# Kernel optimization log

Hardware: AMD Instinct MI355X
Metric: run time of the kernel (lower is better)

Reference implementation:

```python
import jax, jax.numpy as jnp
import numpy as np

EMBED_DIM = 1024
NUM_HEADS = 16
HEAD_DIM = EMBED_DIM // NUM_HEADS


def setup_inputs() -> dict:
    key = jax.random.key(0)
    ks = jax.random.split(key, 5)
    B, S, E = 2, 2048, EMBED_DIM
    # xavier-uniform-ish scale for square linear weights
    lim = float(np.sqrt(6.0 / (E + E)))
    x = jax.random.normal(ks[0], (B, S, E), dtype=jnp.float32)
    Wq = jax.random.uniform(ks[1], (E, E), jnp.float32, -lim, lim)
    Wk = jax.random.uniform(ks[2], (E, E), jnp.float32, -lim, lim)
    Wv = jax.random.uniform(ks[3], (E, E), jnp.float32, -lim, lim)
    Wo = jax.random.uniform(ks[4], (E, E), jnp.float32, -lim, lim)
    z = jnp.zeros((E,), jnp.float32)
    return {"x": x, "Wq": Wq, "bq": z, "Wk": Wk, "bk": z,
            "Wv": Wv, "bv": z, "Wo": Wo, "bo": z}


def reference(x, Wq, bq, Wk, bk, Wv, bv, Wo, bo):
    B, S, E = x.shape
    H, Dh = NUM_HEADS, HEAD_DIM
    # Linear projections (torch Linear: y = x @ W.T + b)
    q = (x @ Wq.T + bq).reshape(B, S, H, Dh).transpose(0, 2, 1, 3)  # [B,H,S,Dh]
    k = (x @ Wk.T + bk).reshape(B, S, H, Dh).transpose(0, 2, 1, 3)
    v = (x @ Wv.T + bv).reshape(B, S, H, Dh).transpose(0, 2, 1, 3)
    # NOTE: module scales by 1/head_dim (not 1/sqrt(head_dim)) — faithful.
    logits = jnp.einsum('bhqd,bhkd->bhqk', q, k) / Dh  # [B,H,S,S]
    attn = jax.nn.softmax(logits, axis=-1)
    vals = jnp.einsum('bhqk,bhkd->bhqd', attn, v)      # [B,H,S,Dh]
    vals = vals.transpose(0, 2, 1, 3).reshape(B, S, E)
    out = vals @ Wo.T + bo
    return out
```

## Files before the change

kernel.cpp:

```cpp
#include <hip/hip_runtime.h>
#include <hip/hip_bf16.h>

#define EDIM 1024
#define NH   16
#define DH   64
#define BB   2
#define SS   2048
#define MM   (BB*SS)

typedef unsigned short u16;
typedef unsigned int   u32;
typedef __attribute__((ext_vector_type(4)))  float f32x4;
typedef __attribute__((ext_vector_type(16))) float f32x16;
typedef __attribute__((ext_vector_type(8)))  short s16x8;

__device__ __forceinline__ u16 f2bf(float x) {
    __hip_bfloat16 b = __float2bfloat16(x);
    return *(u16*)&b;
}
__device__ __forceinline__ u32 cvtpk(float lo, float hi_) {
    u32 r;
    asm("v_cvt_pk_bf16_f32 %0, %1, %2" : "=v"(r) : "v"(lo), "v"(hi_));
    return r;
}
__device__ __forceinline__ void swap32(u32& a, u32& b) {
    asm("v_permlane32_swap_b32 %0, %1" : "+v"(a), "+v"(b));
}

__device__ __forceinline__ void gload16(const void* g, void* l) {
    __builtin_amdgcn_global_load_lds(
        (const __attribute__((address_space(1))) unsigned int*)g,
        (__attribute__((address_space(3))) unsigned int*)l, 16, 0, 0);
}

__global__ __launch_bounds__(256) void convert_all(const float* __restrict__ x,
                                                   const float* __restrict__ Wq,
                                                   const float* __restrict__ Wk,
                                                   const float* __restrict__ Wv,
                                                   const float* __restrict__ Wo,
                                                   u16* __restrict__ xh,
                                                   u16* __restrict__ wqkv,
                                                   u16* __restrict__ woh)
{
    const int i = blockIdx.x * 256 + threadIdx.x;
    const float* src; ushort4* dst; int off;
    if (i < 1048576)      { src = x;  dst = (ushort4*)xh;   off = i; }
    else if (i < 1310720) { src = Wq; dst = (ushort4*)wqkv; off = i - 1048576; }
    else if (i < 1572864) { src = Wk; dst = (ushort4*)wqkv; off = i - 1310720 + 262144; }
    else if (i < 1835008) { src = Wv; dst = (ushort4*)wqkv; off = i - 1572864 + 524288; }
    else                  { src = Wo; dst = (ushort4*)woh;  off = i - 1835008; }
    const int so = (i < 1048576) ? i
                 : (i < 1310720) ? (i - 1048576)
                 : (i < 1572864) ? (i - 1310720)
                 : (i < 1835008) ? (i - 1572864) : (i - 1835008);
    const float4 v = ((const float4*)src)[so];
    ushort4 h;
    h.x = f2bf(v.x); h.y = f2bf(v.y); h.z = f2bf(v.z); h.w = f2bf(v.w);
    dst[off] = h;
}

__global__ __launch_bounds__(256) void gemm_qkv(const u16* __restrict__ A,
                                                const u16* __restrict__ B,
                                                const float* __restrict__ bq,
                                                const float* __restrict__ bk,
                                                const float* __restrict__ bv,
                                                u16* __restrict__ qb,
                                                u16* __restrict__ kb,
                                                u16* __restrict__ vT)
{
    __shared__ __align__(16) u16 As[128][32];
    __shared__ __align__(16) u16 Bs[128][32];

    const int tid  = threadIdx.x;
    const int lane = tid & 63, wid = tid >> 6;
    const int wm = wid >> 1, wn = wid & 1;
    const int swz   = (blockIdx.x & 7) * 96 + (blockIdx.x >> 3);
    const int m0 = (swz & 31) * 128;
    const int n0 = (swz >> 5) * 128;

    f32x4 acc[4][4];
    #pragma unroll
    for (int i = 0; i < 4; ++i)
        #pragma unroll
        for (int j = 0; j < 4; ++j) acc[i][j] = f32x4{0.f, 0.f, 0.f, 0.f};

    const int lrow0 = tid >> 2;
    const int lcol  = (tid & 3) * 8;

    for (int k0 = 0; k0 < 1024; k0 += 32) {
        __syncthreads();
        gload16(A + (size_t)(m0 + lrow0)      * 1024 + k0 + lcol, (char*)As + wid * 1024);
        gload16(A + (size_t)(m0 + 64 + lrow0) * 1024 + k0 + lcol, (char*)As + 4096 + wid * 1024);
        gload16(B + (size_t)(n0 + lrow0)      * 1024 + k0 + lcol, (char*)Bs + wid * 1024);
        gload16(B + (size_t)(n0 + 64 + lrow0) * 1024 + k0 + lcol, (char*)Bs + 4096 + wid * 1024);
        __syncthreads();

        s16x8 af[4], bf[4];
        #pragma unroll
        for (int i = 0; i < 4; ++i) {
            af[i] = *(const s16x8*)&As[wm * 64 + i * 16 + (lane & 15)][(lane >> 4) * 8];
            bf[i] = *(const s16x8*)&Bs[wn * 64 + i * 16 + (lane & 15)][(lane >> 4) * 8];
        }
        #pragma unroll
        for (int i = 0; i < 4; ++i)
            #pragma unroll
            for (int j = 0; j < 4; ++j)
                acc[i][j] = __builtin_amdgcn_mfma_f32_16x16x32_bf16(af[i], bf[j], acc[i][j], 0, 0, 0);
    }

    if (n0 < 1024) {
        #pragma unroll
        for (int i = 0; i < 4; ++i) {
            const int mbase = m0 + wm * 64 + i * 16 + ((lane >> 4) * 4);
            #pragma unroll
            for (int j = 0; j < 4; ++j) {
                const int n = n0 + wn * 64 + j * 16 + (lane & 15);
                const float bias = bq[n];
                const int h_ = n >> 6, d_ = n & 63;
                #pragma unroll
                for (int r = 0; r < 4; ++r) {
                    const int m = mbase + r;
                    const int b_ = m >> 11, s_ = m & 2047;
                    qb[((size_t)(b_ * NH + h_) * SS + s_) * DH + d_] = f2bf(acc[i][j][r] + bias);
                }
            }
        }
    } else if (n0 < 2048) {
        #pragma unroll
        for (int i = 0; i < 4; ++i) {
            const int mbase = m0 + wm * 64 + i * 16 + ((lane >> 4) * 4);
            #pragma unroll
            for (int j = 0; j < 4; ++j) {
                const int n = n0 + wn * 64 + j * 16 + (lane & 15);
                const float bias = bk[n - 1024];
                const int h_ = (n >> 6) & 15, d_ = n & 63;
                #pragma unroll
                for (int r = 0; r < 4; ++r) {
                    const int m = mbase + r;
                    const int b_ = m >> 11, s_ = m & 2047;
                    kb[((size_t)(b_ * NH + h_) * SS + s_) * DH + d_] = f2bf(acc[i][j][r] + bias);
                }
            }
        }
    } else {
        #pragma unroll
        for (int i = 0; i < 4; ++i) {
            const int mbase = m0 + wm * 64 + i * 16 + ((lane >> 4) * 4);
            #pragma unroll
            for (int j = 0; j < 4; ++j) {
                const int n = n0 + wn * 64 + j * 16 + (lane & 15);
                const float bias = bv[n - 2048];
                const int hd = n - 2048;
                #pragma unroll
                for (int r = 0; r < 4; ++r) {
                    const int m = mbase + r;
                    const int b_ = m >> 11, s_ = m & 2047;
                    vT[((size_t)(b_ * EDIM) + hd) * SS + s_] = f2bf(acc[i][j][r] + bias);
                }
            }
        }
    }
}

__global__ __launch_bounds__(256) void gemm_out(const u16* __restrict__ A,
                                                const u16* __restrict__ B,
                                                const float* __restrict__ bo,
                                                float* __restrict__ out)
{
    __shared__ __align__(16) u16 As[64][32];
    __shared__ __align__(16) u16 Bs[128][32];

    const int tid  = threadIdx.x;
    const int lane = tid & 63, wid = tid >> 6;
    const int wm = wid >> 1, wn = wid & 1;
    const int swz = (blockIdx.x & 7) * 64 + (blockIdx.x >> 3);
    const int m0 = (swz & 63) * 64;
    const int n0 = (swz >> 6) * 128;

    f32x4 acc[2][4];
    #pragma unroll
    for (int i = 0; i < 2; ++i)
        #pragma unroll
        for (int j = 0; j < 4; ++j) acc[i][j] = f32x4{0.f, 0.f, 0.f, 0.f};

    const int lrow0 = tid >> 2;
    const int lcol  = (tid & 3) * 8;

    for (int k0 = 0; k0 < 1024; k0 += 32) {
        __syncthreads();
        gload16(A + (size_t)(m0 + lrow0)      * 1024 + k0 + lcol, (char*)As + wid * 1024);
        gload16(B + (size_t)(n0 + lrow0)      * 1024 + k0 + lcol, (char*)Bs + wid * 1024);
        gload16(B + (size_t)(n0 + 64 + lrow0) * 1024 + k0 + lcol, (char*)Bs + 4096 + wid * 1024);
        __syncthreads();

        s16x8 af[2], bf[4];
        #pragma unroll
        for (int i = 0; i < 2; ++i)
            af[i] = *(const s16x8*)&As[wm * 32 + i * 16 + (lane & 15)][(lane >> 4) * 8];
        #pragma unroll
        for (int j = 0; j < 4; ++j)
            bf[j] = *(const s16x8*)&Bs[wn * 64 + j * 16 + (lane & 15)][(lane >> 4) * 8];
        #pragma unroll
        for (int i = 0; i < 2; ++i)
            #pragma unroll
            for (int j = 0; j < 4; ++j)
                acc[i][j] = __builtin_amdgcn_mfma_f32_16x16x32_bf16(af[i], bf[j], acc[i][j], 0, 0, 0);
    }

    #pragma unroll
    for (int i = 0; i < 2; ++i) {
        const int mbase = m0 + wm * 32 + i * 16 + ((lane >> 4) * 4);
        #pragma unroll
        for (int j = 0; j < 4; ++j) {
            const int n = n0 + wn * 64 + j * 16 + (lane & 15);
            #pragma unroll
            for (int r = 0; r < 4; ++r)
                out[(size_t)(mbase + r) * EDIM + n] = acc[i][j][r] + bo[n];
        }
    }
}

__global__ __launch_bounds__(256) void attn_mfma(const u16* __restrict__ q,
                                                 const u16* __restrict__ k,
                                                 const u16* __restrict__ vT,
                                                 u16* __restrict__ valsh)
{
    __shared__ __align__(16) u16 kt[128][64];
    __shared__ __align__(16) u16 vt[64][128];

    const int tid = threadIdx.x, lane = tid & 63, wid = tid >> 6;
    const int lq = lane & 31, hi = lane >> 5;
    const int swz = (blockIdx.x & 7) * 64 + (blockIdx.x >> 3);
    const int bh = swz >> 4, qt = swz & 15;
    const int b = bh >> 4, h = bh & 15;

    const u16* qg = q + ((size_t)bh * SS + qt * 128 + wid * 32 + lq) * DH + hi * 8;
    s16x8 qf[4];
    #pragma unroll
    for (int ks = 0; ks < 4; ++ks) qf[ks] = *(const s16x8*)(qg + ks * 16);

    f32x16 acc_o[2];
    #pragma unroll
    for (int db = 0; db < 2; ++db)
        #pragma unroll
        for (int r = 0; r < 16; ++r) acc_o[db][r] = 0.f;
    float rs = 0.f;

    const char* kbh = (const char*)(k + (size_t)bh * SS * DH);
    const char* vbh = (const char*)(vT + ((size_t)b * EDIM + h * DH) * SS);

    #pragma unroll 1
    for (int c0 = 0; c0 < SS; c0 += 128) {
        #pragma unroll
        for (int i = 0; i < 4; ++i) {
            const int flat = i * 256 + tid;
            const int row = flat >> 3, u = flat & 7;
            gload16(kbh + (size_t)(c0 + row) * 128 + ((u ^ (row & 7)) << 4),
                    (char*)kt + (i * 256 + wid * 64) * 16);
        }
        #pragma unroll
        for (int i = 0; i < 4; ++i) {
            const int flat = i * 256 + tid;
            const int row = flat >> 4, u = flat & 15;
            gload16(vbh + (size_t)row * (SS * 2) + (size_t)c0 * 2 + ((u ^ (row & 15)) << 4),
                    (char*)vt + (i * 256 + wid * 64) * 16);
        }
        __syncthreads();

        #pragma unroll
        for (int kb = 0; kb < 4; ++kb) {
            f32x16 sc;
            #pragma unroll
            for (int r = 0; r < 16; ++r) sc[r] = 0.f;
            const int krow = kb * 32 + lq;
            __builtin_amdgcn_s_setprio(1);
            #pragma unroll
            for (int ks = 0; ks < 4; ++ks) {
                const int u = (ks * 2 + hi) ^ (krow & 7);
                const s16x8 kf = *(const s16x8*)((const char*)kt + krow * 128 + u * 16);
                sc = __builtin_amdgcn_mfma_f32_32x32x16_bf16(kf, qf[ks], sc, 0, 0, 0);
            }
            __builtin_amdgcn_s_setprio(0);

            #pragma unroll
            for (int r = 0; r < 16; ++r) {
                sc[r] = __builtin_amdgcn_exp2f(sc[r] * 0.0225421209f);
                rs += sc[r];
            }

            u32 w0 = cvtpk(sc[0],  sc[1]),  w1 = cvtpk(sc[2],  sc[3]);
            u32 w2 = cvtpk(sc[4],  sc[5]),  w3 = cvtpk(sc[6],  sc[7]);
            u32 w4 = cvtpk(sc[8],  sc[9]),  w5 = cvtpk(sc[10], sc[11]);
            u32 w6 = cvtpk(sc[12], sc[13]), w7 = cvtpk(sc[14], sc[15]);
            swap32(w0, w2);
            swap32(w1, w3);
            swap32(w4, w6);
            swap32(w5, w7);
            union { u32 w[4]; s16x8 v; } pa0, pa1;
            pa0.w[0] = w0; pa0.w[1] = w1; pa0.w[2] = w2; pa0.w[3] = w3;
            pa1.w[0] = w4; pa1.w[1] = w5; pa1.w[2] = w6; pa1.w[3] = w7;

            __builtin_amdgcn_s_setprio(1);
            #pragma unroll
            for (int t = 0; t < 2; ++t) {
                const s16x8 pat = t ? pa1.v : pa0.v;
                const int kst = kb * 2 + t;
                #pragma unroll
                for (int db = 0; db < 2; ++db) {
                    const int vrow = db * 32 + lq;
                    const int u = (kst * 2 + hi) ^ (vrow & 15);
                    const s16x8 vf = *(const s16x8*)((const char*)vt + vrow * 256 + u * 16);
                    acc_o[db] = __builtin_amdgcn_mfma_f32_32x32x16_bf16(pat, vf, acc_o[db], 0, 0, 0);
                }
            }
            __builtin_amdgcn_s_setprio(0);
        }
        __syncthreads();
    }

    const float rsf = rs + __shfl_xor(rs, 32, 64);
    const float inv = 1.f / rsf;
    float iv[16];
    #pragma unroll
    for (int r = 0; r < 16; ++r)
        iv[r] = __shfl(inv, (r & 3) + 8 * (r >> 2) + 4 * hi, 64);

    #pragma unroll
    for (int db = 0; db < 2; ++db)
        #pragma unroll
        for (int r = 0; r < 16; ++r) {
            const int srow = qt * 128 + wid * 32 + (r & 3) + 8 * (r >> 2) + 4 * hi;
            const int col  = h * 64 + db * 32 + lq;
            valsh[(size_t)(b * SS + srow) * EDIM + col] = f2bf(acc_o[db][r] * iv[r]);
        }
}

extern "C" void kernel_launch(void* const* d_in, const int* in_sizes, int n_in,
                              void* d_out, int out_size, void* d_ws, size_t ws_size,
                              hipStream_t stream)
{
    const float* x  = (const float*)d_in[0];
    const float* Wq = (const float*)d_in[1];
    const float* bq = (const float*)d_in[2];
    const float* Wk = (const float*)d_in[3];
    const float* bk = (const float*)d_in[4];
    const float* Wv = (const float*)d_in[5];
    const float* bv = (const float*)d_in[6];
    const float* Wo = (const float*)d_in[7];
    const float* bo = (const float*)d_in[8];
    float* out = (float*)d_out;

    u16* W = (u16*)d_ws;
    const size_t M1 = 1024 * 1024;
    u16* xh    = W;
    u16* wqkv  = W + 4  * M1;
    u16* woh   = W + 7  * M1;
    u16* qbuf  = W + 8  * M1;
    u16* kbuf  = W + 12 * M1;
    u16* vbufT = W + 16 * M1;
    u16* valsh = W + 20 * M1;

    convert_all<<<dim3(8192), 256, 0, stream>>>(x, Wq, Wk, Wv, Wo, xh, wqkv, woh);

    gemm_qkv<<<dim3(768), 256, 0, stream>>>(xh, wqkv, bq, bk, bv, qbuf, kbuf, vbufT);

    attn_mfma<<<dim3(BB * NH * (SS / 128)), 256, 0, stream>>>(qbuf, kbuf, vbufT, valsh);

    gemm_out<<<dim3(512), 256, 0, stream>>>(valsh, woh, bo, out);
}
```

Before: 205.2 us.

## Double-buffer LDS tiles in GEMMs and attention with swizzled, deeper K tiles

Adds two-stage LDS double buffering to the QKV projection, output projection and attention kernels, so the async global-to-LDS loads for the next tile are issued before computing on the current one. Each iteration then needs one barrier instead of two. The GEMMs also widen the K step from 32 to 64 and XOR-swizzle the LDS layout to avoid bank conflicts. In exchange, LDS use doubles, which may lower occupancy, and the swizzle adds some address arithmetic.

```diff
diff --git a/kernel.cpp b/kernel.cpp
--- a/kernel.cpp
+++ b/kernel.cpp
@@ -68,45 +68,71 @@
                                                 u16* __restrict__ kb,
                                                 u16* __restrict__ vT)
 {
-    __shared__ __align__(16) u16 As[128][32];
-    __shared__ __align__(16) u16 Bs[128][32];
+    __shared__ __align__(16) u16 As[2][128][64];
+    __shared__ __align__(16) u16 Bs[2][128][64];
 
     const int tid  = threadIdx.x;
     const int lane = tid & 63, wid = tid >> 6;
     const int wm = wid >> 1, wn = wid & 1;
-    const int swz   = (blockIdx.x & 7) * 96 + (blockIdx.x >> 3);
+    const int swz = (blockIdx.x & 7) * 96 + (blockIdx.x >> 3);
     const int m0 = (swz & 31) * 128;
     const int n0 = (swz >> 5) * 128;
 
+    const char* Abase = (const char*)(A + (size_t)m0 * 1024);
+    const char* Bbase = (const char*)(B + (size_t)n0 * 1024);
+
     f32x4 acc[4][4];
     #pragma unroll
     for (int i = 0; i < 4; ++i)
         #pragma unroll
         for (int j = 0; j < 4; ++j) acc[i][j] = f32x4{0.f, 0.f, 0.f, 0.f};
 
-    const int lrow0 = tid >> 2;
-    const int lcol  = (tid & 3) * 8;
-
-    for (int k0 = 0; k0 < 1024; k0 += 32) {
+    auto stage = [&](int buf, int k0) {
+        #pragma unroll
+        for (int i = 0; i < 4; ++i) {
+            const int flat = i * 256 + tid;
+            const int row = flat >> 3, u = flat & 7;
+            const size_t so = (size_t)row * 2048 + (size_t)k0 * 2 + ((u ^ (row & 7)) << 4);
+            gload16(Abase + so, (char*)As + buf * 16384 + (i * 256 + wid * 64) * 16);
+        }
+        #pragma unroll
+        for (int i = 0; i < 4; ++i) {
+            const int flat = i * 256 + tid;
+            const int row = flat >> 3, u = flat & 7;
+            const size_t so = (size_t)row * 2048 + (size_t)k0 * 2 + ((u ^ (row & 7)) << 4);
+            gload16(Bbase + so, (char*)Bs + buf * 16384 + (i * 256 + wid * 64) * 16);
+        }
+    };
+    auto compute = [&](int buf) {
+        const char* Ab = (const char*)As + buf * 16384;
+        const char* Bb = (const char*)Bs + buf * 16384;
+        #pragma unroll
+        for (int kk = 0; kk < 2; ++kk) {
+            s16x8 af[4], bfr[4];
+            #pragma unroll
+            for (int i = 0; i < 4; ++i) {
+                const int rowA = wm * 64 + i * 16 + (lane & 15);
+                af[i] = *(const s16x8*)(Ab + rowA * 128 + (((kk * 4 + (lane >> 4)) ^ (rowA & 7)) << 4));
+                const int rowB = wn * 64 + i * 16 + (lane & 15);
+                bfr[i] = *(const s16x8*)(Bb + rowB * 128 + (((kk * 4 + (lane >> 4)) ^ (rowB & 7)) << 4));
+            }
+            #pragma unroll
+            for (int i = 0; i < 4; ++i)
+                #pragma unroll
+                for (int j = 0; j < 4; ++j)
+                    acc[i][j] = __builtin_amdgcn_mfma_f32_16x16x32_bf16(af[i], bfr[j], acc[i][j], 0, 0, 0);
+        }
+    };
+
+    stage(0, 0);
+    __syncthreads();
+    #pragma unroll 1
+    for (int t = 0; t < 15; ++t) {
+        stage((t & 1) ^ 1, (t + 1) * 64);
+        compute(t & 1);
         __syncthreads();
-        gload16(A + (size_t)(m0 + lrow0)      * 1024 + k0 + lcol, (char*)As + wid * 1024);
-        gload16(A + (size_t)(m0 + 64 + lrow0) * 1024 + k0 + lcol, (char*)As + 4096 + wid * 1024);
-        gload16(B + (size_t)(n0 + lrow0)      * 1024 + k0 + lcol, (char*)Bs + wid * 1024);
-        gload16(B + (size_t)(n0 + 64 + lrow0) * 1024 + k0 + lcol, (char*)Bs + 4096 + wid * 1024);
-        __syncthreads();
-
-        s16x8 af[4], bf[4];
-        #pragma unroll
-        for (int i = 0; i < 4; ++i) {
-            af[i] = *(const s16x8*)&As[wm * 64 + i * 16 + (lane & 15)][(lane >> 4) * 8];
-            bf[i] = *(const s16x8*)&Bs[wn * 64 + i * 16 + (lane & 15)][(lane >> 4) * 8];
-        }
-        #pragma unroll
-        for (int i = 0; i < 4; ++i)
-            #pragma unroll
-            for (int j = 0; j < 4; ++j)
-                acc[i][j] = __builtin_amdgcn_mfma_f32_16x16x32_bf16(af[i], bf[j], acc[i][j], 0, 0, 0);
     }
+    compute(1);
 
     if (n0 < 1024) {
         #pragma unroll
@@ -167,8 +193,8 @@
                                                 const float* __restrict__ bo,
                                                 float* __restrict__ out)
 {
-    __shared__ __align__(16) u16 As[64][32];
-    __shared__ __align__(16) u16 Bs[128][32];
+    __shared__ __align__(16) u16 As[2][64][64];
+    __shared__ __align__(16) u16 Bs[2][128][64];
 
     const int tid  = threadIdx.x;
     const int lane = tid & 63, wid = tid >> 6;
@@ -177,35 +203,64 @@
     const int m0 = (swz & 63) * 64;
     const int n0 = (swz >> 6) * 128;
 
+    const char* Abase = (const char*)(A + (size_t)m0 * 1024);
+    const char* Bbase = (const char*)(B + (size_t)n0 * 1024);
+
     f32x4 acc[2][4];
     #pragma unroll
     for (int i = 0; i < 2; ++i)
         #pragma unroll
         for (int j = 0; j < 4; ++j) acc[i][j] = f32x4{0.f, 0.f, 0.f, 0.f};
 
-    const int lrow0 = tid >> 2;
-    const int lcol  = (tid & 3) * 8;
-
-    for (int k0 = 0; k0 < 1024; k0 += 32) {
+    auto stage = [&](int buf, int k0) {
+        #pragma unroll
+        for (int i = 0; i < 2; ++i) {
+            const int flat = i * 256 + tid;
+            const int row = flat >> 3, u = flat & 7;
+            const size_t so = (size_t)row * 2048 + (size_t)k0 * 2 + ((u ^ (row & 7)) << 4);
+            gload16(Abase + so, (char*)As + buf * 8192 + (i * 256 + wid * 64) * 16);
+        }
+        #pragma unroll
+        for (int i = 0; i < 4; ++i) {
+            const int flat = i * 256 + tid;
+            const int row = flat >> 3, u = flat & 7;
+            const size_t so = (size_t)row * 2048 + (size_t)k0 * 2 + ((u ^ (row & 7)) << 4);
+            gload16(Bbase + so, (char*)Bs + buf * 16384 + (i * 256 + wid * 64) * 16);
+        }
+    };
+    auto compute = [&](int buf) {
+        const char* Ab = (const char*)As + buf * 8192;
+        const char* Bb = (const char*)Bs + buf * 16384;
+        #pragma unroll
+        for (int kk = 0; kk < 2; ++kk) {
+            s16x8 af[2], bfr[4];
+            #pragma unroll
+            for (int i = 0; i < 2; ++i) {
+                const int rowA = wm * 32 + i * 16 + (lane & 15);
+                af[i] = *(const s16x8*)(Ab + rowA * 128 + (((kk * 4 + (lane >> 4)) ^ (rowA & 7)) << 4));
+            }
+            #pragma unroll
+            for (int j = 0; j < 4; ++j) {
+                const int rowB = wn * 64 + j * 16 + (lane & 15);
+                bfr[j] = *(const s16x8*)(Bb + rowB * 128 + (((kk * 4 + (lane >> 4)) ^ (rowB & 7)) << 4));
+            }
+            #pragma unroll
+            for (int i = 0; i < 2; ++i)
+                #pragma unroll
+                for (int j = 0; j < 4; ++j)
+                    acc[i][j] = __builtin_amdgcn_mfma_f32_16x16x32_bf16(af[i], bfr[j], acc[i][j], 0, 0, 0);
+        }
+    };
+
+    stage(0, 0);
+    __syncthreads();
+    #pragma unroll 1
+    for (int t = 0; t < 15; ++t) {
+        stage((t & 1) ^ 1, (t + 1) * 64);
+        compute(t & 1);
         __syncthreads();
-        gload16(A + (size_t)(m0 + lrow0)      * 1024 + k0 + lcol, (char*)As + wid * 1024);
-        gload16(B + (size_t)(n0 + lrow0)      * 1024 + k0 + lcol, (char*)Bs + wid * 1024);
-        gload16(B + (size_t)(n0 + 64 + lrow0) * 1024 + k0 + lcol, (char*)Bs + 4096 + wid * 1024);
-        __syncthreads();
-
-        s16x8 af[2], bf[4];
-        #pragma unroll
-        for (int i = 0; i < 2; ++i)
-            af[i] = *(const s16x8*)&As[wm * 32 + i * 16 + (lane & 15)][(lane >> 4) * 8];
-        #pragma unroll
-        for (int j = 0; j < 4; ++j)
-            bf[j] = *(const s16x8*)&Bs[wn * 64 + j * 16 + (lane & 15)][(lane >> 4) * 8];
-        #pragma unroll
-        for (int i = 0; i < 2; ++i)
-            #pragma unroll
-            for (int j = 0; j < 4; ++j)
-                acc[i][j] = __builtin_amdgcn_mfma_f32_16x16x32_bf16(af[i], bf[j], acc[i][j], 0, 0, 0);
     }
+    compute(1);
 
     #pragma unroll
     for (int i = 0; i < 2; ++i) {
@@ -225,8 +280,8 @@
                                                  const u16* __restrict__ vT,
                                                  u16* __restrict__ valsh)
 {
-    __shared__ __align__(16) u16 kt[128][64];
-    __shared__ __align__(16) u16 vt[64][128];
+    __shared__ __align__(16) u16 kt[2][128][64];
+    __shared__ __align__(16) u16 vt[2][64][128];
 
     const int tid = threadIdx.x, lane = tid & 63, wid = tid >> 6;
     const int lq = lane & 31, hi = lane >> 5;
@@ -249,23 +304,32 @@
     const char* kbh = (const char*)(k + (size_t)bh * SS * DH);
     const char* vbh = (const char*)(vT + ((size_t)b * EDIM + h * DH) * SS);
 
-    #pragma unroll 1
-    for (int c0 = 0; c0 < SS; c0 += 128) {
+    auto stage = [&](int buf, int c0) {
         #pragma unroll
         for (int i = 0; i < 4; ++i) {
             const int flat = i * 256 + tid;
             const int row = flat >> 3, u = flat & 7;
             gload16(kbh + (size_t)(c0 + row) * 128 + ((u ^ (row & 7)) << 4),
-                    (char*)kt + (i * 256 + wid * 64) * 16);
+                    (char*)kt + buf * 16384 + (i * 256 + wid * 64) * 16);
         }
         #pragma unroll
         for (int i = 0; i < 4; ++i) {
             const int flat = i * 256 + tid;
             const int row = flat >> 4, u = flat & 15;
             gload16(vbh + (size_t)row * (SS * 2) + (size_t)c0 * 2 + ((u ^ (row & 15)) << 4),
-                    (char*)vt + (i * 256 + wid * 64) * 16);
-        }
-        __syncthreads();
+                    (char*)vt + buf * 16384 + (i * 256 + wid * 64) * 16);
+        }
+    };
+
+    stage(0, 0);
+    __syncthreads();
+
+    int buf = 0;
+    #pragma unroll 1
+    for (int c = 0; c < 16; ++c) {
+        if (c < 15) stage(buf ^ 1, (c + 1) * 128);
+        const char* ktb = (const char*)kt + buf * 16384;
+        const char* vtb = (const char*)vt + buf * 16384;
 
         #pragma unroll
         for (int kb = 0; kb < 4; ++kb) {
@@ -277,7 +341,7 @@
             #pragma unroll
             for (int ks = 0; ks < 4; ++ks) {
                 const int u = (ks * 2 + hi) ^ (krow & 7);
-                const s16x8 kf = *(const s16x8*)((const char*)kt + krow * 128 + u * 16);
+                const s16x8 kf = *(const s16x8*)(ktb + krow * 128 + u * 16);
                 sc = __builtin_amdgcn_mfma_f32_32x32x16_bf16(kf, qf[ks], sc, 0, 0, 0);
             }
             __builtin_amdgcn_s_setprio(0);
@@ -309,13 +373,14 @@
                 for (int db = 0; db < 2; ++db) {
                     const int vrow = db * 32 + lq;
                     const int u = (kst * 2 + hi) ^ (vrow & 15);
-                    const s16x8 vf = *(const s16x8*)((const char*)vt + vrow * 256 + u * 16);
+                    const s16x8 vf = *(const s16x8*)(vtb + vrow * 256 + u * 16);
                     acc_o[db] = __builtin_amdgcn_mfma_f32_32x32x16_bf16(pat, vf, acc_o[db], 0, 0, 0);
                 }
             }
             __builtin_amdgcn_s_setprio(0);
         }
         __syncthreads();
+        buf ^= 1;
     }
 
     const float rsf = rs + __shfl_xor(rs, 32, 64);
```

Result: slower. 210.6 us (+2.7%).
